# Kernel optimization log

Hardware: AMD Instinct MI355X
Metric: run time of the kernel (lower is better)

## Reference

```python
import jax, jax.numpy as jnp
import numpy as np

B, T, S, D = 4, 2048, 4, 1024
SINKHORN_ITERS = 20
EPS = 1e-8


def sinkhorn(matrix, iterations=SINKHORN_ITERS, eps=EPS):
    # Project onto doubly stochastic matrices via alternating normalization.
    P = jnp.exp(matrix - jnp.max(matrix, axis=-1, keepdims=True))
    def body(_, P):
        P = P / (jnp.sum(P, axis=-1, keepdims=True) + eps)
        P = P / (jnp.sum(P, axis=-2, keepdims=True) + eps)
        return P
    return jax.lax.fori_loop(0, iterations, body, P)


def setup_inputs() -> dict:
    key = jax.random.key(0)
    k1, k2, k3 = jax.random.split(key, 3)
    x = jax.random.normal(k1, (B, T, S, D), dtype=jnp.float32)
    layer_output = jax.random.normal(k2, (B, T, D), dtype=jnp.float32)
    H_res = jax.random.normal(k3, (S, S), dtype=jnp.float32) * 0.01
    H_pos = jnp.full((S, 1), 1.0 / S, dtype=jnp.float32)
    alpha_res = jnp.float32(0.01)
    alpha_pos = jnp.float32(0.01)
    bias_res = jnp.zeros((S, D), dtype=jnp.float32)
    bias_pos = jnp.zeros((S, D), dtype=jnp.float32)
    return {"x": x, "layer_output": layer_output, "H_res": H_res,
            "H_pos": H_pos, "alpha_res": alpha_res, "alpha_pos": alpha_pos,
            "bias_res": bias_res, "bias_pos": bias_pos}


def reference(x, layer_output, H_res, H_pos, alpha_res, alpha_pos, bias_res, bias_pos):
    H_res_proj = sinkhorn(H_res)  # (S, S) doubly stochastic
    # mix streams: [B,T,S,D] x [S,R] -> [B,T,R,D]
    x_mixed = jnp.einsum('btsd,sr->btrd', x, H_res_proj)
    x_mixed = alpha_res * x_mixed + bias_res[None, None, :, :]
    # broadcast layer output across streams, scaled per-stream by H_pos
    layer_out = layer_output[:, :, None, :] * H_pos[None, None, :, :]  # (B,T,S,D)
    layer_out = alpha_pos * layer_out + bias_pos[None, None, :, :]
    return x + x_mixed + layer_out
```

## Files before the change

### kernel.cpp

```cpp
#include <hip/hip_runtime.h>
#include <hip/hip_bf16.h>

constexpr int Bc = 4;
constexpr int Tc = 2048;
constexpr int Sc = 4;
constexpr int Dc = 1024;
constexpr int BT = Bc * Tc;
constexpr int SD = Sc * Dc;
constexpr int SINKHORN_ITERS = 20;

constexpr int WS_CB_BYTE_OFF = 128;

__global__ void prep_kernel(const float* __restrict__ Hres,
                            const float* __restrict__ Hpos,
                            const float* __restrict__ alpha_res,
                            const float* __restrict__ alpha_pos,
                            const float* __restrict__ bias_res,
                            const float* __restrict__ bias_pos,
                            float* __restrict__ ws_f,
                            float* __restrict__ ws_cb) {
    const int tid = threadIdx.x;
    if (tid == 0) {
        float P[4][4];
        for (int i = 0; i < 4; ++i) {
            float row[4];
            float m = -3.0e38f;
            for (int j = 0; j < 4; ++j) {
                row[j] = Hres[i * 4 + j];
                m = fmaxf(m, row[j]);
            }
            for (int j = 0; j < 4; ++j) P[i][j] = __expf(row[j] - m);
        }
        for (int it = 0; it < SINKHORN_ITERS; ++it) {
            for (int i = 0; i < 4; ++i) {
                float s = P[i][0] + P[i][1] + P[i][2] + P[i][3] + 1e-8f;
                float r = 1.0f / s;
                for (int j = 0; j < 4; ++j) P[i][j] *= r;
            }
            for (int j = 0; j < 4; ++j) {
                float s = P[0][j] + P[1][j] + P[2][j] + P[3][j] + 1e-8f;
                float r = 1.0f / s;
                for (int i = 0; i < 4; ++i) P[i][j] *= r;
            }
        }
        const float ar = alpha_res[0];
        const float ap = alpha_pos[0];
        for (int r = 0; r < 4; ++r)
            for (int s = 0; s < 4; ++s)
                ws_f[r * 4 + s] = ar * P[s][r];
        for (int r = 0; r < 4; ++r)
            ws_f[16 + r] = ap * Hpos[r];
    }
    for (int i = tid; i < SD; i += blockDim.x)
        ws_cb[i] = bias_res[i] + bias_pos[i];
}

__global__ __launch_bounds__(256) void main_kernel(
        const float* __restrict__ x,
        const float* __restrict__ lo,
        const float* __restrict__ ws_f,
        const float* __restrict__ ws_cb,
        float* __restrict__ out) {
    const int idx = blockIdx.x * 256 + threadIdx.x;
    const int bt  = idx >> 8;
    const int d0  = (idx & 255) << 2;

    const float4 aH0 = reinterpret_cast<const float4*>(ws_f)[0];
    const float4 aH1 = reinterpret_cast<const float4*>(ws_f)[1];
    const float4 aH2 = reinterpret_cast<const float4*>(ws_f)[2];
    const float4 aH3 = reinterpret_cast<const float4*>(ws_f)[3];
    const float4 hp  = reinterpret_cast<const float4*>(ws_f)[4];
    const float aH[4][4] = {{aH0.x, aH0.y, aH0.z, aH0.w},
                            {aH1.x, aH1.y, aH1.z, aH1.w},
                            {aH2.x, aH2.y, aH2.z, aH2.w},
                            {aH3.x, aH3.y, aH3.z, aH3.w}};
    const float hpr[4] = {hp.x, hp.y, hp.z, hp.w};

    const int xbase = bt * SD + d0;

    float xs[4][4];
#pragma unroll
    for (int s = 0; s < 4; ++s) {
        const float4 v = *reinterpret_cast<const float4*>(x + xbase + s * Dc);
        xs[s][0] = v.x; xs[s][1] = v.y; xs[s][2] = v.z; xs[s][3] = v.w;
    }
    const float4 lv = *reinterpret_cast<const float4*>(lo + bt * Dc + d0);
    const float lf[4] = {lv.x, lv.y, lv.z, lv.w};

#pragma unroll
    for (int r = 0; r < 4; ++r) {
        const float4 cbv = *reinterpret_cast<const float4*>(ws_cb + r * Dc + d0);
        const float cb[4] = {cbv.x, cbv.y, cbv.z, cbv.w};
        float acc[4];
#pragma unroll
        for (int j = 0; j < 4; ++j)
            acc[j] = fmaf(lf[j], hpr[r], xs[r][j] + cb[j]);
#pragma unroll
        for (int s = 0; s < 4; ++s)
#pragma unroll
            for (int j = 0; j < 4; ++j)
                acc[j] = fmaf(xs[s][j], aH[r][s], acc[j]);
        float4 o;
        o.x = acc[0]; o.y = acc[1]; o.z = acc[2]; o.w = acc[3];
        *reinterpret_cast<float4*>(out + xbase + r * Dc) = o;
    }
}

extern "C" void kernel_launch(void* const* d_in, const int* in_sizes, int n_in,
                              void* d_out, int out_size, void* d_ws, size_t ws_size,
                              hipStream_t stream) {
    const float* x         = (const float*)d_in[0];
    const float* layer_out = (const float*)d_in[1];
    const float* H_res     = (const float*)d_in[2];
    const float* H_pos     = (const float*)d_in[3];
    const float* alpha_res = (const float*)d_in[4];
    const float* alpha_pos = (const float*)d_in[5];
    const float* bias_res  = (const float*)d_in[6];
    const float* bias_pos  = (const float*)d_in[7];
    float* out = (float*)d_out;

    float* ws_f  = (float*)d_ws;
    float* ws_cb = (float*)((char*)d_ws + WS_CB_BYTE_OFF);

    prep_kernel<<<1, 256, 0, stream>>>(H_res, H_pos, alpha_res, alpha_pos,
                                       bias_res, bias_pos, ws_f, ws_cb);

    const int nthreads = BT * (Dc / 4);
    main_kernel<<<nthreads / 256, 256, 0, stream>>>(x, layer_out, ws_f, ws_cb, out);
}
```

Measured before the change: 275.5 us.

## Fuse Sinkhorn prep into main kernel with per-block shuffle reduction and nontemporal stores

Removes the separate single-block prep kernel. Each block now recomputes the 4x4 Sinkhorn projection in 16 lanes using cross-lane shuffles, shares the result through LDS, and adds the two bias vectors inline. Output stores are marked nontemporal. This saves one kernel launch and the serial single-thread prep, at the cost of redundant Sinkhorn work and a __syncthreads in every block plus extra bias loads.

```diff
diff --git a/kernel.cpp b/kernel.cpp
--- a/kernel.cpp
+++ b/kernel.cpp
@@ -9,88 +9,67 @@
 constexpr int SD = Sc * Dc;
 constexpr int SINKHORN_ITERS = 20;
 
-constexpr int WS_CB_BYTE_OFF = 128;
+typedef float vfloat4 __attribute__((ext_vector_type(4)));
 
-__global__ void prep_kernel(const float* __restrict__ Hres,
-                            const float* __restrict__ Hpos,
-                            const float* __restrict__ alpha_res,
-                            const float* __restrict__ alpha_pos,
-                            const float* __restrict__ bias_res,
-                            const float* __restrict__ bias_pos,
-                            float* __restrict__ ws_f,
-                            float* __restrict__ ws_cb) {
-    const int tid = threadIdx.x;
-    if (tid == 0) {
-        float P[4][4];
-        for (int i = 0; i < 4; ++i) {
-            float row[4];
-            float m = -3.0e38f;
-            for (int j = 0; j < 4; ++j) {
-                row[j] = Hres[i * 4 + j];
-                m = fmaxf(m, row[j]);
-            }
-            for (int j = 0; j < 4; ++j) P[i][j] = __expf(row[j] - m);
-        }
-        for (int it = 0; it < SINKHORN_ITERS; ++it) {
-            for (int i = 0; i < 4; ++i) {
-                float s = P[i][0] + P[i][1] + P[i][2] + P[i][3] + 1e-8f;
-                float r = 1.0f / s;
-                for (int j = 0; j < 4; ++j) P[i][j] *= r;
-            }
-            for (int j = 0; j < 4; ++j) {
-                float s = P[0][j] + P[1][j] + P[2][j] + P[3][j] + 1e-8f;
-                float r = 1.0f / s;
-                for (int i = 0; i < 4; ++i) P[i][j] *= r;
-            }
-        }
-        const float ar = alpha_res[0];
-        const float ap = alpha_pos[0];
-        for (int r = 0; r < 4; ++r)
-            for (int s = 0; s < 4; ++s)
-                ws_f[r * 4 + s] = ar * P[s][r];
-        for (int r = 0; r < 4; ++r)
-            ws_f[16 + r] = ap * Hpos[r];
-    }
-    for (int i = tid; i < SD; i += blockDim.x)
-        ws_cb[i] = bias_res[i] + bias_pos[i];
-}
-
-__global__ __launch_bounds__(256) void main_kernel(
+__global__ __launch_bounds__(256) void fused_kernel(
         const float* __restrict__ x,
         const float* __restrict__ lo,
-        const float* __restrict__ ws_f,
-        const float* __restrict__ ws_cb,
+        const float* __restrict__ Hres,
+        const float* __restrict__ Hpos,
+        const float* __restrict__ alpha_res,
+        const float* __restrict__ alpha_pos,
+        const float* __restrict__ bias_res,
+        const float* __restrict__ bias_pos,
         float* __restrict__ out) {
-    const int idx = blockIdx.x * 256 + threadIdx.x;
-    const int bt  = idx >> 8;
-    const int d0  = (idx & 255) << 2;
+    __shared__ float s_aH[16];
+    __shared__ float s_hp[4];
 
-    const float4 aH0 = reinterpret_cast<const float4*>(ws_f)[0];
-    const float4 aH1 = reinterpret_cast<const float4*>(ws_f)[1];
-    const float4 aH2 = reinterpret_cast<const float4*>(ws_f)[2];
-    const float4 aH3 = reinterpret_cast<const float4*>(ws_f)[3];
-    const float4 hp  = reinterpret_cast<const float4*>(ws_f)[4];
-    const float aH[4][4] = {{aH0.x, aH0.y, aH0.z, aH0.w},
-                            {aH1.x, aH1.y, aH1.z, aH1.w},
-                            {aH2.x, aH2.y, aH2.z, aH2.w},
-                            {aH3.x, aH3.y, aH3.z, aH3.w}};
-    const float hpr[4] = {hp.x, hp.y, hp.z, hp.w};
+    const int tid = threadIdx.x;
+    if (tid < 16) {
+        const int i = tid >> 2;
+        const int j = tid & 3;
+        const float h = Hres[i * 4 + j];
+        float m = fmaxf(h, __shfl_xor(h, 1));
+        m = fmaxf(m, __shfl_xor(m, 2));
+        float P = __expf(h - m);
+        for (int it = 0; it < SINKHORN_ITERS; ++it) {
+            float s = P + __shfl_xor(P, 1);
+            s += __shfl_xor(s, 2);
+            P = P / (s + 1e-8f);
+            float c = P + __shfl_xor(P, 4);
+            c += __shfl_xor(c, 8);
+            P = P / (c + 1e-8f);
+        }
+        s_aH[j * 4 + i] = alpha_res[0] * P;
+        if (i == 0) s_hp[j] = alpha_pos[0] * Hpos[j];
+    }
+    __syncthreads();
 
+    float aH[4][4];
+#pragma unroll
+    for (int r = 0; r < 4; ++r)
+#pragma unroll
+        for (int s = 0; s < 4; ++s) aH[r][s] = s_aH[r * 4 + s];
+    const float hpr[4] = {s_hp[0], s_hp[1], s_hp[2], s_hp[3]};
+
+    const int bt = blockIdx.x;
+    const int d0 = tid << 2;
     const int xbase = bt * SD + d0;
 
     float xs[4][4];
 #pragma unroll
     for (int s = 0; s < 4; ++s) {
-        const float4 v = *reinterpret_cast<const float4*>(x + xbase + s * Dc);
+        const vfloat4 v = *reinterpret_cast<const vfloat4*>(x + xbase + s * Dc);
         xs[s][0] = v.x; xs[s][1] = v.y; xs[s][2] = v.z; xs[s][3] = v.w;
     }
-    const float4 lv = *reinterpret_cast<const float4*>(lo + bt * Dc + d0);
+    const vfloat4 lv = *reinterpret_cast<const vfloat4*>(lo + bt * Dc + d0);
     const float lf[4] = {lv.x, lv.y, lv.z, lv.w};
 
 #pragma unroll
     for (int r = 0; r < 4; ++r) {
-        const float4 cbv = *reinterpret_cast<const float4*>(ws_cb + r * Dc + d0);
-        const float cb[4] = {cbv.x, cbv.y, cbv.z, cbv.w};
+        const vfloat4 br = *reinterpret_cast<const vfloat4*>(bias_res + r * Dc + d0);
+        const vfloat4 bp = *reinterpret_cast<const vfloat4*>(bias_pos + r * Dc + d0);
+        const float cb[4] = {br.x + bp.x, br.y + bp.y, br.z + bp.z, br.w + bp.w};
         float acc[4];
 #pragma unroll
         for (int j = 0; j < 4; ++j)
@@ -100,9 +79,9 @@
 #pragma unroll
             for (int j = 0; j < 4; ++j)
                 acc[j] = fmaf(xs[s][j], aH[r][s], acc[j]);
-        float4 o;
+        vfloat4 o;
         o.x = acc[0]; o.y = acc[1]; o.z = acc[2]; o.w = acc[3];
-        *reinterpret_cast<float4*>(out + xbase + r * Dc) = o;
+        __builtin_nontemporal_store(o, reinterpret_cast<vfloat4*>(out + xbase + r * Dc));
     }
 }
 
@@ -119,12 +98,7 @@
     const float* bias_pos  = (const float*)d_in[7];
     float* out = (float*)d_out;
 
-    float* ws_f  = (float*)d_ws;
-    float* ws_cb = (float*)((char*)d_ws + WS_CB_BYTE_OFF);
-
-    prep_kernel<<<1, 256, 0, stream>>>(H_res, H_pos, alpha_res, alpha_pos,
-                                       bias_res, bias_pos, ws_f, ws_cb);
-
-    const int nthreads = BT * (Dc / 4);
-    main_kernel<<<nthreads / 256, 256, 0, stream>>>(x, layer_out, ws_f, ws_cb, out);
+    fused_kernel<<<BT, 256, 0, stream>>>(x, layer_out, H_res, H_pos,
+                                         alpha_res, alpha_pos,
+                                         bias_res, bias_pos, out);
 }
```

New measurement: 269.6 us. 1.02x faster.
